# Performance work log

Measured on AMD Instinct MI355X. Metric: run time of the kernel, lower is better.

Reference implementation:

```python
import jax, jax.numpy as jnp
import numpy as np
from jax import lax

EPS = 1e-6

def _haar_weights():
    w = jnp.array([[[1, 1], [1, 1]],
                   [[1, -1], [1, -1]],
                   [[1, 1], [-1, -1]],
                   [[1, -1], [-1, 1]]], dtype=jnp.float32) / 2.0
    return w[:, None, :, :]  # [4,1,2,2] OIHW


def setup_inputs() -> dict:
    key = jax.random.key(0)
    x = jax.random.uniform(key, (256, 3, 224, 224), dtype=jnp.float32)
    return {
        "x": x,
        "haar_weights": _haar_weights(),
        "mean": jnp.array([0.485, 0.456, 0.406], jnp.float32).reshape(1, 3, 1, 1),
        "std": jnp.array([0.229, 0.224, 0.225], jnp.float32).reshape(1, 3, 1, 1),
    }


def _conv(x, w, stride=1, padding='VALID'):
    return lax.conv_general_dilated(
        x, w, window_strides=(stride, stride), padding=padding,
        dimension_numbers=('NCHW', 'OIHW', 'NCHW'))


def _minmax_norm(v):
    return (v - v.min()) / (v.max() - v.min() + EPS)


def _wavelet_boost(xs, haar_w):
    # xs: [B,1,H,W]; Haar analysis via stride-2 2x2 conv -> [B,4,H/2,W/2]
    coeffs = _conv(xs, haar_w, stride=2, padding='VALID')
    gains = jnp.array([0.1, 2.5, 2.5, 3.5], jnp.float32).reshape(1, 4, 1, 1)
    scaled = coeffs * gains
    # conv_transpose2d stride 2, 2x2 kernel == scatter each coeff to a 2x2 block
    B, _, Hh, Wh = scaled.shape
    rec = jnp.einsum('bchw,cokl->bohkwl', scaled, haar_w)  # [B,1,H/2,2,W/2,2]
    rec = rec.reshape(B, 1, Hh * 2, Wh * 2)
    return _minmax_norm(rec)


def _ridge_enhancement(xs):
    kx = jnp.array([[-1, 0, 1], [-2, 0, 2], [-1, 0, 1]], jnp.float32)[None, None]
    ky = jnp.array([[-1, -2, -1], [0, 0, 0], [1, 2, 1]], jnp.float32)[None, None]
    ix = _conv(xs, kx, padding='SAME')
    iy = _conv(xs, ky, padding='SAME')
    ixx = _conv(ix, kx, padding='SAME')
    iyy = _conv(iy, ky, padding='SAME')
    vesselness = jnp.abs(ixx + iyy)
    return _minmax_norm(vesselness)


def reference(x, haar_weights, mean, std):
    structural = x[:, 0:1, :, :]                  # [B,1,H,W]
    frequency = _wavelet_boost(structural, haar_weights)
    ridge = _ridge_enhancement(structural)
    combined = jnp.concatenate([structural, frequency, ridge], axis=1)  # [B,3,H,W]
    return (combined - mean) / std
```

## Files before the change

kernel.cpp:

```cpp
#include <hip/hip_runtime.h>

#define IMG 224
#define PLANE (IMG * IMG)
#define BANDROWS 14
#define NBANDS 16
#define NWAVES (256 * NBANDS)
#define NPBLK (NWAVES / 4)

typedef float fl4 __attribute__((ext_vector_type(4)));

__device__ __forceinline__ unsigned int ford(float f) {
    unsigned int u = __float_as_uint(f);
    return (u & 0x80000000u) ? ~u : (u | 0x80000000u);
}
__device__ __forceinline__ float funord(unsigned int u) {
    unsigned int v = (u & 0x80000000u) ? (u & 0x7FFFFFFFu) : ~u;
    return __uint_as_float(v);
}

template<bool WRITE>
__global__ __launch_bounds__(256)
void band_kernel(const float* __restrict__ x, float* __restrict__ out,
                 uint4* __restrict__ partials, const unsigned int* __restrict__ red)
{
    const int wid  = (blockIdx.x << 2) + (threadIdx.x >> 6);
    const int lane = threadIdx.x & 63;
    const int img  = wid >> 4;
    const int band = wid & 15;
    const int r0   = band * BANDROWS;
    const bool active = lane < 56;
    const int col = lane * 4;
    const float* xp = x + (size_t)img * 3 * PLANE;

    float rmin = 0.f, rsc = 0.f, vmin = 0.f, vsc = 0.f;
    if constexpr (WRITE) {
        rmin = funord(red[0]); const float rmax = funord(red[1]);
        vmin = funord(red[2]); const float vmax = funord(red[3]);
        rsc = 1.f / (rmax - rmin + 1e-6f);
        vsc = 1.f / (vmax - vmin + 1e-6f);
    }
    const float m0 = 0.485f, i0 = 1.f / 0.229f;
    const float m1 = 0.456f, i1 = 1.f / 0.224f;
    const float m2 = 0.406f, i2 = 1.f / 0.225f;

    float rmn = 3.4e38f, rmx = -3.4e38f, vmn = 3.4e38f, vmx = -3.4e38f;

    auto loadrow = [&](int gr) -> fl4 {
        fl4 v = (fl4)0.f;
        if (active && (unsigned)gr < (unsigned)IMG)
            v = *(const fl4*)(xp + gr * IMG + col);
        return v;
    };

    auto pref = [&](fl4 p, fl4& uu, fl4& ww) {
        float cl1 = __shfl_up(p[3], 1);
        float cl2 = __shfl_up(p[2], 1);
        float cr1 = __shfl_down(p[0], 1);
        float cr2 = __shfl_down(p[1], 1);
        if (lane == 0) { cl1 = 0.f; cl2 = 0.f; }
        uu[0] = cl2 - 2.f*p[0] + p[2];
        uu[1] = cl1 - 2.f*p[1] + p[3];
        uu[2] = p[0] - 2.f*p[2] + cr1;
        uu[3] = p[1] - 2.f*p[3] + cr2;
        ww[0] = cl2 + 4.f*cl1 + 6.f*p[0] + 4.f*p[1] + p[2];
        ww[1] = cl1 + 4.f*p[0] + 6.f*p[1] + 4.f*p[2] + p[3];
        ww[2] = p[0] + 4.f*p[1] + 6.f*p[2] + 4.f*p[3] + cr1;
        ww[3] = p[1] + 4.f*p[2] + 6.f*p[3] + 4.f*cr1 + cr2;
    };

    auto haar2 = [&](fl4 xe, fl4 xo, fl4& re_, fl4& ro_) {
        #pragma unroll
        for (int q = 0; q < 2; ++q) {
            const float a = xe[2*q], b = xe[2*q+1], c = xo[2*q], d = xo[2*q+1];
            const float h0 = (a+b+c+d)*0.5f, h1 = (a-b+c-d)*0.5f;
            const float h2 = (a+b-c-d)*0.5f, h3 = (a-b-c+d)*0.5f;
            const float s0 = 0.1f*h0, s1 = 2.5f*h1, s2 = 2.5f*h2, s3 = 3.5f*h3;
            re_[2*q]   = (s0+s1+s2+s3)*0.5f;
            re_[2*q+1] = (s0-s1+s2-s3)*0.5f;
            ro_[2*q]   = (s0+s1-s2-s3)*0.5f;
            ro_[2*q+1] = (s0-s1-s2+s3)*0.5f;
        }
    };

    auto dorow = [&](int gr, fl4 ua, fl4 ub, fl4 uc, fl4 ud, fl4 ue,
                     fl4 wa, fl4 wb, fl4 wc, fl4 wd, fl4 we,
                     fl4 pm1, fl4 p0c, fl4 pp1, fl4 recv) {
        fl4 t;
        #pragma unroll
        for (int j = 0; j < 4; ++j)
            t[j] = ua[j] + 4.f*ub[j] + 6.f*uc[j] + 4.f*ud[j] + ue[j]
                 + wa[j] - 2.f*wc[j] + we[j];
        const bool rb = (gr == 0) | (gr == IMG - 1);
        if (rb) {
            #pragma unroll
            for (int j = 0; j < 4; ++j) t[j] -= (uc[j] - wc[j]);
        }
        const float corr0 = -4.f*(pm1[0] + 2.f*p0c[0] + pp1[0]);
        const float corr3 = -4.f*(pm1[3] + 2.f*p0c[3] + pp1[3]);
        if (lane == 0)  t[0] -= corr0 + (rb ? 2.f*p0c[0] : 0.f);
        if (lane == 55) t[3] -= corr3 + (rb ? 2.f*p0c[3] : 0.f);
        fl4 ves;
        #pragma unroll
        for (int j = 0; j < 4; ++j) ves[j] = fabsf(t[j]);

        if (active) {
            #pragma unroll
            for (int j = 0; j < 4; ++j) {
                rmn = fminf(rmn, recv[j]); rmx = fmaxf(rmx, recv[j]);
                vmn = fminf(vmn, ves[j]);  vmx = fmaxf(vmx, ves[j]);
            }
            if constexpr (WRITE) {
                float* op = out + (size_t)img * 3 * PLANE + gr * IMG + col;
                fl4 o0, o1, o2;
                #pragma unroll
                for (int j = 0; j < 4; ++j) {
                    o0[j] = (p0c[j] - m0) * i0;
                    o1[j] = ((recv[j] - rmin) * rsc - m1) * i1;
                    o2[j] = ((ves[j]  - vmin) * vsc - m2) * i2;
                }
                *(fl4*)op               = o0;
                *(fl4*)(op + PLANE)     = o1;
                *(fl4*)(op + 2 * PLANE) = o2;
            }
        }
    };

    fl4 uA, uB, uC, uD, wA, wB, wC, wD, pB, pC, pD;
    {
        fl4 pA = loadrow(r0 - 2); pref(pA, uA, wA);
        pB = loadrow(r0 - 1); pref(pB, uB, wB);
        pC = loadrow(r0);     pref(pC, uC, wC);
        pD = loadrow(r0 + 1); pref(pD, uD, wD);
    }

    for (int k = 0; k < 7; ++k) {
        const int re = r0 + 2 * k;
        fl4 pE = loadrow(re + 2); fl4 uE, wE; pref(pE, uE, wE);
        fl4 rec_e, rec_o; haar2(pC, pD, rec_e, rec_o);
        dorow(re,     uA, uB, uC, uD, uE, wA, wB, wC, wD, wE, pB, pC, pD, rec_e);
        fl4 pF = loadrow(re + 3); fl4 uF, wF; pref(pF, uF, wF);
        dorow(re + 1, uB, uC, uD, uE, uF, wB, wC, wD, wE, wF, pC, pD, pE, rec_o);
        uA = uC; uB = uD; uC = uE; uD = uF;
        wA = wC; wB = wD; wC = wE; wD = wF;
        pB = pD; pC = pE; pD = pF;
    }

    if constexpr (!WRITE) {
        #pragma unroll
        for (int off = 32; off; off >>= 1) {
            rmn = fminf(rmn, __shfl_down(rmn, off));
            rmx = fmaxf(rmx, __shfl_down(rmx, off));
            vmn = fminf(vmn, __shfl_down(vmn, off));
            vmx = fmaxf(vmx, __shfl_down(vmx, off));
        }
        __shared__ uint4 wred[4];
        if (lane == 0) {
            uint4 p;
            p.x = ford(rmn); p.y = ford(rmx); p.z = ford(vmn); p.w = ford(vmx);
            wred[threadIdx.x >> 6] = p;
        }
        __syncthreads();
        if (threadIdx.x == 0) {
            uint4 p = wred[0];
            #pragma unroll
            for (int w = 1; w < 4; ++w) {
                p.x = min(p.x, wred[w].x); p.y = max(p.y, wred[w].y);
                p.z = min(p.z, wred[w].z); p.w = max(p.w, wred[w].w);
            }
            partials[blockIdx.x] = p;
        }
    }
}

__global__ __launch_bounds__(256)
void reduce_partials(const uint4* __restrict__ partials, unsigned int* __restrict__ red)
{
    __shared__ unsigned int wred[4][4];
    const int tid = threadIdx.x;
    unsigned int mn0 = 0xFFFFFFFFu, mx1 = 0u, mn2 = 0xFFFFFFFFu, mx3 = 0u;
    for (int i = tid; i < NPBLK; i += 256) {
        uint4 p = partials[i];
        mn0 = min(mn0, p.x); mx1 = max(mx1, p.y);
        mn2 = min(mn2, p.z); mx3 = max(mx3, p.w);
    }
    #pragma unroll
    for (int off = 32; off; off >>= 1) {
        mn0 = min(mn0, (unsigned)__shfl_down((int)mn0, off));
        mx1 = max(mx1, (unsigned)__shfl_down((int)mx1, off));
        mn2 = min(mn2, (unsigned)__shfl_down((int)mn2, off));
        mx3 = max(mx3, (unsigned)__shfl_down((int)mx3, off));
    }
    const int wave = tid >> 6;
    if ((tid & 63) == 0) {
        wred[wave][0] = mn0; wred[wave][1] = mx1;
        wred[wave][2] = mn2; wred[wave][3] = mx3;
    }
    __syncthreads();
    if (tid == 0) {
        unsigned int a0 = wred[0][0], a1 = wred[0][1], a2 = wred[0][2], a3 = wred[0][3];
        #pragma unroll
        for (int w = 1; w < 4; ++w) {
            a0 = min(a0, wred[w][0]); a1 = max(a1, wred[w][1]);
            a2 = min(a2, wred[w][2]); a3 = max(a3, wred[w][3]);
        }
        red[0] = a0; red[1] = a1; red[2] = a2; red[3] = a3;
    }
}

extern "C" void kernel_launch(void* const* d_in, const int* in_sizes, int n_in,
                              void* d_out, int out_size, void* d_ws, size_t ws_size,
                              hipStream_t stream) {
    const float* x = (const float*)d_in[0];
    float* out = (float*)d_out;
    unsigned int* red = (unsigned int*)d_ws;
    uint4* partials = (uint4*)((char*)d_ws + 64);

    band_kernel<false><<<dim3(NPBLK), 256, 0, stream>>>(x, nullptr, partials, nullptr);
    reduce_partials<<<1, 256, 0, stream>>>(partials, red);
    band_kernel<true ><<<dim3(NPBLK), 256, 0, stream>>>(x, out, nullptr, red);
}
```

Baseline: 61.34 us.

## Cache fp16 intermediates in workspace and replace recompute pass with affine kernel

```diff
diff --git a/kernel.cpp b/kernel.cpp
--- a/kernel.cpp
+++ b/kernel.cpp
@@ -1,4 +1,5 @@
 #include <hip/hip_runtime.h>
+#include <hip/hip_fp16.h>
 
 #define IMG 224
 #define PLANE (IMG * IMG)
@@ -6,8 +7,12 @@
 #define NBANDS 16
 #define NWAVES (256 * NBANDS)
 #define NPBLK (NWAVES / 4)
+#define GROUPS_PER_IMG (PLANE / 4)
 
 typedef float fl4 __attribute__((ext_vector_type(4)));
+
+#define WS_CMB_OFF 65536
+#define WS_NEED (WS_CMB_OFF + (size_t)256 * PLANE * 4)
 
 __device__ __forceinline__ unsigned int ford(float f) {
     unsigned int u = __float_as_uint(f);
@@ -18,10 +23,11 @@
     return __uint_as_float(v);
 }
 
-template<bool WRITE>
+template<int MODE>
 __global__ __launch_bounds__(256)
 void band_kernel(const float* __restrict__ x, float* __restrict__ out,
-                 uint4* __restrict__ partials, const unsigned int* __restrict__ red)
+                 uint4* __restrict__ cmb4, uint4* __restrict__ partials,
+                 const unsigned int* __restrict__ red)
 {
     const int wid  = (blockIdx.x << 2) + (threadIdx.x >> 6);
     const int lane = threadIdx.x & 63;
@@ -33,7 +39,7 @@
     const float* xp = x + (size_t)img * 3 * PLANE;
 
     float rmin = 0.f, rsc = 0.f, vmin = 0.f, vsc = 0.f;
-    if constexpr (WRITE) {
+    if constexpr (MODE == 2) {
         rmin = funord(red[0]); const float rmax = funord(red[1]);
         vmin = funord(red[2]); const float vmax = funord(red[3]);
         rsc = 1.f / (rmax - rmin + 1e-6f);
@@ -109,7 +115,20 @@
                 rmn = fminf(rmn, recv[j]); rmx = fmaxf(rmx, recv[j]);
                 vmn = fminf(vmn, ves[j]);  vmx = fmaxf(vmx, ves[j]);
             }
-            if constexpr (WRITE) {
+            if constexpr (MODE == 1) {
+                float* op = out + (size_t)img * 3 * PLANE + gr * IMG + col;
+                fl4 o0;
+                #pragma unroll
+                for (int j = 0; j < 4; ++j) o0[j] = (p0c[j] - m0) * i0;
+                *(fl4*)op = o0;
+                uint4 c;
+                c.x = __builtin_bit_cast(unsigned int, __floats2half2_rn(recv[0], recv[1]));
+                c.y = __builtin_bit_cast(unsigned int, __floats2half2_rn(recv[2], recv[3]));
+                c.z = __builtin_bit_cast(unsigned int, __floats2half2_rn(ves[0], ves[1]));
+                c.w = __builtin_bit_cast(unsigned int, __floats2half2_rn(ves[2], ves[3]));
+                cmb4[(size_t)img * GROUPS_PER_IMG + gr * (IMG / 4) + lane] = c;
+            }
+            if constexpr (MODE == 2) {
                 float* op = out + (size_t)img * 3 * PLANE + gr * IMG + col;
                 fl4 o0, o1, o2;
                 #pragma unroll
@@ -145,7 +164,7 @@
         pB = pD; pC = pE; pD = pF;
     }
 
-    if constexpr (!WRITE) {
+    if constexpr (MODE != 2) {
         #pragma unroll
         for (int off = 32; off; off >>= 1) {
             rmn = fminf(rmn, __shfl_down(rmn, off));
@@ -207,6 +226,42 @@
     }
 }
 
+__global__ __launch_bounds__(256)
+void affine_kernel(const uint4* __restrict__ cmb4, float* __restrict__ out,
+                   const unsigned int* __restrict__ red)
+{
+    const int g   = blockIdx.x * 256 + threadIdx.x;
+    const int img = g / GROUPS_PER_IMG;
+    const int o4  = g - img * GROUPS_PER_IMG;
+
+    const float rmin = funord(red[0]), rmax = funord(red[1]);
+    const float vmin = funord(red[2]), vmax = funord(red[3]);
+    const float rsc = 1.f / (rmax - rmin + 1e-6f);
+    const float vsc = 1.f / (vmax - vmin + 1e-6f);
+    const float m1 = 0.456f, i1 = 1.f / 0.224f;
+    const float m2 = 0.406f, i2 = 1.f / 0.225f;
+
+    const uint4 c = cmb4[g];
+    const float2 r01 = __half22float2(__builtin_bit_cast(__half2, c.x));
+    const float2 r23 = __half22float2(__builtin_bit_cast(__half2, c.y));
+    const float2 v01 = __half22float2(__builtin_bit_cast(__half2, c.z));
+    const float2 v23 = __half22float2(__builtin_bit_cast(__half2, c.w));
+
+    fl4 o1, o2;
+    o1[0] = ((r01.x - rmin) * rsc - m1) * i1;
+    o1[1] = ((r01.y - rmin) * rsc - m1) * i1;
+    o1[2] = ((r23.x - rmin) * rsc - m1) * i1;
+    o1[3] = ((r23.y - rmin) * rsc - m1) * i1;
+    o2[0] = ((v01.x - vmin) * vsc - m2) * i2;
+    o2[1] = ((v01.y - vmin) * vsc - m2) * i2;
+    o2[2] = ((v23.x - vmin) * vsc - m2) * i2;
+    o2[3] = ((v23.y - vmin) * vsc - m2) * i2;
+
+    float* base = out + (size_t)img * 3 * PLANE + PLANE + o4 * 4;
+    *(fl4*)base           = o1;
+    *(fl4*)(base + PLANE) = o2;
+}
+
 extern "C" void kernel_launch(void* const* d_in, const int* in_sizes, int n_in,
                               void* d_out, int out_size, void* d_ws, size_t ws_size,
                               hipStream_t stream) {
@@ -214,8 +269,15 @@
     float* out = (float*)d_out;
     unsigned int* red = (unsigned int*)d_ws;
     uint4* partials = (uint4*)((char*)d_ws + 64);
-
-    band_kernel<false><<<dim3(NPBLK), 256, 0, stream>>>(x, nullptr, partials, nullptr);
-    reduce_partials<<<1, 256, 0, stream>>>(partials, red);
-    band_kernel<true ><<<dim3(NPBLK), 256, 0, stream>>>(x, out, nullptr, red);
-}
+    uint4* cmb4 = (uint4*)((char*)d_ws + WS_CMB_OFF);
+
+    if (ws_size >= WS_NEED) {
+        band_kernel<1><<<dim3(NPBLK), 256, 0, stream>>>(x, out, cmb4, partials, nullptr);
+        reduce_partials<<<1, 256, 0, stream>>>(partials, red);
+        affine_kernel<<<dim3(256 * GROUPS_PER_IMG / 256), 256, 0, stream>>>(cmb4, out, red);
+    } else {
+        band_kernel<0><<<dim3(NPBLK), 256, 0, stream>>>(x, nullptr, nullptr, partials, nullptr);
+        reduce_partials<<<1, 256, 0, stream>>>(partials, red);
+        band_kernel<2><<<dim3(NPBLK), 256, 0, stream>>>(x, out, nullptr, nullptr, red);
+    }
+}
```

After: 66.78 us. +8.9%, slower.
